# Performance work log

Measured on AMD Instinct MI355X. Metric: run time of the kernel, lower is better.

## Reference

```python
import jax, jax.numpy as jnp
import numpy as np

HEADS = 6
HEAD_DIM = 64  # channels // heads = 384 // 6
R = 2          # sparse sampler stride


def setup_inputs() -> dict:
    key = jax.random.key(0)
    k1, k2 = jax.random.split(key)
    x = jax.random.normal(k1, (8, 384, 96, 96), dtype=jnp.float32)
    # 1x1 conv weight, no bias: (out_ch=3*C, in_ch=C)
    w_qkv = jax.random.normal(k2, (1152, 384), dtype=jnp.float32) * 0.02
    return {"x": x, "w_qkv": w_qkv}


def reference(x, w_qkv):
    # sparse sampler: AvgPool2d(kernel_size=1, stride=R) == strided subsampling
    xs = x[:, :, ::R, ::R]                       # [B, C, H', W']
    B, C, H, W = xs.shape
    N = H * W
    # fused 1x1 conv producing qkv: [B, 3C, H', W']
    qkv = jnp.einsum('bchw,oc->bohw', xs, w_qkv)
    qkv = qkv.reshape(B, HEADS, 3 * HEAD_DIM, N)  # [B, h, 3d, N]
    q, k, v = jnp.split(qkv, 3, axis=2)           # each [B, h, d, N]
    # attn = (q^T @ k).softmax(-1)  -- NOTE: original forward applies no scale
    attn = jax.nn.softmax(jnp.einsum('bhdn,bhdm->bhnm', q, k), axis=-1)  # [B,h,N,N]
    # out = v @ attn^T -> [B, h, d, N]
    out = jnp.einsum('bhdm,bhnm->bhdn', v, attn)
    return out.reshape(B, C, H, W)
```

## Files before the change

### kernel.cpp

```cpp
#include <hip/hip_runtime.h>


#define NTOK 2304
#define NB 8
#define W_U16 (1152 * 384)
#define XT_U16 (NTOK * 384)
#define PLANE_U16 (NTOK * 64)
#define KVTILE_U16 8192
#define HEAD_U16 (PLANE_U16 + 36 * KVTILE_U16)
#define SLOT_U16 (XT_U16 + 6 * HEAD_U16)
#define SLOT_BYTES ((size_t)SLOT_U16 * 2)
#define WBYTES ((size_t)W_U16 * 2)
#define LOG2E 1.4426950408889634f
#define WSCALE 1024.0f
#define WS_INV (1.0f / 1024.0f)
#define SM_OFF 8.0f

typedef __attribute__((ext_vector_type(8))) _Float16 f16x8;
typedef __attribute__((ext_vector_type(4))) float f32x4;

__device__ __forceinline__ ushort f2h(float f) {
  union { _Float16 h; ushort u; } v; v.h = (_Float16)f; return v.u;
}
__device__ __forceinline__ uint cvt_pk_f16(float lo, float hi) {
  uint r;
  asm("v_cvt_pkrtz_f16_f32 %0, %1, %2" : "=v"(r) : "v"(lo), "v"(hi));
  return r;
}
__device__ __forceinline__ float exp2_fast(float x) {
  float r;
  asm("v_exp_f32 %0, %1" : "=v"(r) : "v"(x));
  return r;
}

__global__ __launch_bounds__(256) void prep_w_kernel(
    const float* __restrict__ w, ushort* __restrict__ wsu) {
  const int idx4 = blockIdx.x * 256 + threadIdx.x;
  const int o = idx4 / 96;
  const float scale = (((o % 192) < 64) ? LOG2E : 1.0f) * WSCALE;
  float4 v = *(const float4*)&w[(size_t)idx4 * 4];
  uint2 uh;
  uh.x = (uint)f2h(v.x * scale) | ((uint)f2h(v.y * scale) << 16);
  uh.y = (uint)f2h(v.z * scale) | ((uint)f2h(v.w * scale) << 16);
  *(uint2*)&wsu[(size_t)idx4 * 4] = uh;
}

__global__ __launch_bounds__(256) void prep_x_kernel(
    const float* __restrict__ x, ushort* __restrict__ wsu, int b0) {
  const int hh = blockIdx.x, cc = blockIdx.y, bb = blockIdx.z;
  const int b = b0 + bb;
  const int c0 = cc * 64;
  ushort* xth = wsu + (size_t)W_U16 + (size_t)bb * SLOT_U16;
  const float* xb = x + ((size_t)b * 384 + c0) * 9216 + 192 * hh;

  __shared__ float T[64][49];
  const int tid = threadIdx.x;
#pragma unroll
  for (int i = 0; i < 8; ++i) {
    int idx = tid + 256 * i;
    int cl = idx >> 5, q = idx & 31;
    if (q < 24) {
      float4 v = *(const float4*)&xb[(size_t)cl * 9216 + 4 * q];
      T[cl][2 * q] = v.x;
      T[cl][2 * q + 1] = v.z;
    }
  }
  __syncthreads();
#pragma unroll
  for (int i = 0; i < 2; ++i) {
    int item = tid + 256 * i;
    if (item < 384) {
      int ww = item >> 3, cg = item & 7;
      int n = hh * 48 + ww;
      uint uh[4];
#pragma unroll
      for (int p = 0; p < 4; ++p) {
        float f0 = T[8 * cg + 2 * p][ww], f1 = T[8 * cg + 2 * p + 1][ww];
        uh[p] = (uint)f2h(f0) | ((uint)f2h(f1) << 16);
      }
      uint4 H = {uh[0], uh[1], uh[2], uh[3]};
      *(uint4*)&xth[(size_t)n * 384 + c0 + 8 * cg] = H;
    }
  }
}

__global__ __launch_bounds__(256) void qkv_mfma_kernel(
    const ushort* __restrict__ wsu, int b0) {
  const int nT = blockIdx.x, oT = blockIdx.y, bb = blockIdx.z;
  const ushort* whi = wsu;
  const ushort* slot = wsu + (size_t)W_U16 + (size_t)bb * SLOT_U16;
  const ushort* xth = slot;
  const int oBase = oT * 64, nBase = nT * 64;

  __shared__ __align__(16) ushort Wh[64 * 64];
  __shared__ __align__(16) ushort Xh[64 * 64];

  const int tid = threadIdx.x;
  const int w = tid >> 6, l = tid & 63;
  const int lq = l & 15, lh = l >> 4;

  const int r0 = tid >> 3, g0 = tid & 7;
  const size_t srcA = (size_t)(oBase + r0) * 384 + 8 * g0;
  const size_t srcB = (size_t)(nBase + r0) * 384 + 8 * g0;
  const int dst0 = r0 * 64 + 8 * (g0 ^ (r0 & 7));
  const int dst1 = dst0 + 2048;

  f32x4 acc[4];
#pragma unroll
  for (int f = 0; f < 4; ++f) acc[f] = (f32x4){0.f, 0.f, 0.f, 0.f};

  uint4 t0, t1, t2, t3;
#define QSTAGE(c0)                                                        \
  {                                                                       \
    t0 = *(const uint4*)&whi[srcA + (c0)];                                \
    t1 = *(const uint4*)&whi[srcA + 32 * 384 + (c0)];                     \
    t2 = *(const uint4*)&xth[srcB + (c0)];                                \
    t3 = *(const uint4*)&xth[srcB + 32 * 384 + (c0)];                     \
  }
#define QCOMMIT()                                                         \
  {                                                                       \
    *(uint4*)&Wh[dst0] = t0; *(uint4*)&Wh[dst1] = t1;                     \
    *(uint4*)&Xh[dst0] = t2; *(uint4*)&Xh[dst1] = t3;                     \
  }

  QSTAGE(0)
  for (int step = 0; step < 6; ++step) {
    QCOMMIT()
    __syncthreads();
    if (step < 5) QSTAGE((step + 1) * 64)
    __builtin_amdgcn_s_setprio(1);
#pragma unroll
    for (int s = 0; s < 2; ++s) {
      const int nrow = 16 * w + lq;
      const int g = 4 * s + lh;
      f16x8 xh = *(const f16x8*)&Xh[nrow * 64 + 8 * (g ^ (nrow & 7))];
#pragma unroll
      for (int f = 0; f < 4; ++f) {
        const int orow = 16 * f + lq;
        f16x8 wh_ = *(const f16x8*)&Wh[orow * 64 + 8 * (g ^ (orow & 7))];
        acc[f] = __builtin_amdgcn_mfma_f32_16x16x32_f16(wh_, xh, acc[f], 0, 0, 0);
      }
    }
    __builtin_amdgcn_s_setprio(0);
    __syncthreads();
  }

  const int t = oT % 3, head = oT / 3;
  ushort* pb = (ushort*)slot + (size_t)XT_U16 + (size_t)head * HEAD_U16;
  if (t == 0) {
    const int n = nBase + 16 * w + lq;
#pragma unroll
    for (int f = 0; f < 4; ++f) {
      uint2 uh;
      uh.x = (uint)f2h(acc[f][0] * WS_INV) | ((uint)f2h(acc[f][1] * WS_INV) << 16);
      uh.y = (uint)f2h(acc[f][2] * WS_INV) | ((uint)f2h(acc[f][3] * WS_INV) << 16);
      *(uint2*)&pb[(size_t)n * 64 + 16 * f + 4 * lh] = uh;
    }
  } else if (t == 1) {
    ushort* kv = pb + (size_t)PLANE_U16 + (size_t)nT * KVTILE_U16;
    const int row = 16 * w + lq;
#pragma unroll
    for (int f = 0; f < 4; ++f) {
      uint2 uh;
      uh.x = (uint)f2h(acc[f][0] * WS_INV) | ((uint)f2h(acc[f][1] * WS_INV) << 16);
      uh.y = (uint)f2h(acc[f][2] * WS_INV) | ((uint)f2h(acc[f][3] * WS_INV) << 16);
      const int idx = row * 64 + 8 * ((2 * f + (lh >> 1)) ^ (row & 7)) + 4 * (lh & 1);
      *(uint2*)&kv[idx] = uh;
    }
  } else {
    ushort* pv = pb + (size_t)PLANE_U16 + (size_t)nT * KVTILE_U16 + 4096;
    const int col = 16 * w + lq;
    const int cg = col >> 3, cr = col & 7;
#pragma unroll
    for (int f = 0; f < 4; ++f)
#pragma unroll
      for (int r = 0; r < 4; ++r) {
        const int row = 16 * f + 4 * lh + r;
        pv[row * 64 + 8 * (cg ^ (row & 7)) + cr] = f2h(acc[f][r] * WS_INV);
      }
  }
}

__global__ __launch_bounds__(256, 5) void attn_mfma_kernel(
    const ushort* __restrict__ wsu, float* __restrict__ out, int b0, int nbw) {
  int wid = blockIdx.x + 36 * (blockIdx.y + 6 * blockIdx.z);
  const int nwg = 36 * 6 * nbw;
  if ((nwg & 7) == 0) {
    const int chunk = nwg >> 3;
    wid = (wid & 7) * chunk + (wid >> 3);
  }
  const int qt = wid % 36;
  const int rest = wid / 36;
  const int h = rest % 6;
  const int bb = rest / 6;
  const int b = b0 + bb;

  const ushort* pbh = wsu + (size_t)W_U16 + (size_t)bb * SLOT_U16 +
                      (size_t)XT_U16 + (size_t)h * HEAD_U16;
  const ushort* qhP = pbh;
  const char* kvG = (const char*)(pbh + (size_t)PLANE_U16);
  const int n0 = qt * 64;

  __shared__ __align__(16) ushort KV[8192];
  __shared__ __align__(16) ushort Pw[4][16 * 64];

  const int tid = threadIdx.x;
  const int w = tid >> 6;
  const int l = tid & 63;
  const int lq = l & 15;
  const int lh = l >> 4;

  f16x8 qh[2];
  {
    const int qrow = n0 + 16 * w + lq;
    const ushort* qr = qhP + (size_t)qrow * 64 + 8 * lh;
    qh[0] = *(const f16x8*)(qr);
    qh[1] = *(const f16x8*)(qr + 32);
  }

  f32x4 oac[4];
#pragma unroll
  for (int i = 0; i < 4; ++i) oac[i] = (f32x4){0.f, 0.f, 0.f, 0.f};
  float l_lane = 0.f;

  const char* gbase = kvG + w * 4096 + l * 16;
  char* lbase = (char*)&KV[0] + w * 4096 + l * 16;

  uint4 s0, s1, s2, s3;
#define ASTAGE(mt)                                                        \
  {                                                                       \
    const char* p_ = gbase + (size_t)(mt) * 16384;                        \
    s0 = *(const uint4*)(p_);                                             \
    s1 = *(const uint4*)(p_ + 1024);                                      \
    s2 = *(const uint4*)(p_ + 2048);                                      \
    s3 = *(const uint4*)(p_ + 3072);                                      \
  }
#define ACOMMIT()                                                         \
  {                                                                       \
    *(uint4*)(lbase) = s0;                                                \
    *(uint4*)(lbase + 1024) = s1;                                         \
    *(uint4*)(lbase + 2048) = s2;                                         \
    *(uint4*)(lbase + 3072) = s3;                                         \
  }

  ASTAGE(0)
  ACOMMIT()
  __syncthreads();

  const ushort* Kh = &KV[0];
  const ushort* Vh = &KV[4096];

  for (int mt = 0; mt < 36; ++mt) {
    const bool hasNext = (mt + 1 < 36);
    if (hasNext) ASTAGE(mt + 1)

    f32x4 st[4];
#pragma unroll
    for (int f = 0; f < 4; ++f) st[f] = (f32x4){0.f, 0.f, 0.f, 0.f};
    __builtin_amdgcn_s_setprio(1);
#pragma unroll
    for (int f = 0; f < 4; ++f) {
#pragma unroll
      for (int s = 0; s < 2; ++s) {
        const int row = 16 * f + lq;
        const int g = 4 * s + lh;
        f16x8 kh = *(const f16x8*)&Kh[row * 64 + 8 * (g ^ (row & 7))];
        st[f] = __builtin_amdgcn_mfma_f32_16x16x32_f16(kh, qh[s], st[f], 0, 0, 0);
      }
    }
    __builtin_amdgcn_s_setprio(0);

#pragma unroll
    for (int f = 0; f < 4; ++f)
#pragma unroll
      for (int r = 0; r < 4; ++r) {
        st[f][r] = exp2_fast(st[f][r] - SM_OFF);
        l_lane += st[f][r];
      }

    ushort* pw = &Pw[w][0];
#pragma unroll
    for (int f = 0; f < 4; ++f) {
      uint2 uu;
      uu.x = cvt_pk_f16(st[f][0], st[f][1]);
      uu.y = cvt_pk_f16(st[f][2], st[f][3]);
      int ui = lq * 64 + 8 * ((2 * f + (lh >> 1)) ^ (lq & 7)) + 4 * (lh & 1);
      *(uint2*)&pw[ui] = uu;
    }
    f16x8 pbf[2];
#pragma unroll
    for (int s = 0; s < 2; ++s)
      pbf[s] = *(const f16x8*)&pw[lq * 64 + 8 * ((4 * s + lh) ^ (lq & 7))];

    __builtin_amdgcn_s_setprio(1);
#pragma unroll
    for (int fd = 0; fd < 4; ++fd) {
#pragma unroll
      for (int s = 0; s < 2; ++s) {
        const int row = 16 * fd + lq;
        const int g = 4 * s + lh;
        f16x8 av = *(const f16x8*)&Vh[row * 64 + 8 * (g ^ (row & 7))];
        oac[fd] = __builtin_amdgcn_mfma_f32_16x16x32_f16(av, pbf[s], oac[fd], 0, 0, 0);
      }
    }
    __builtin_amdgcn_s_setprio(0);

    if (hasNext) {
      __syncthreads();
      ACOMMIT()
      __syncthreads();
    }
  }

  float lt = l_lane;
  lt += __shfl_xor(lt, 16);
  lt += __shfl_xor(lt, 32);
  const float inv = 1.f / lt;

  const int ncol = n0 + 16 * w + lq;
#pragma unroll
  for (int fd = 0; fd < 4; ++fd)
#pragma unroll
    for (int r = 0; r < 4; ++r)
      out[((size_t)b * 384 + h * 64 + 16 * fd + 4 * lh + r) * NTOK + ncol] =
          oac[fd][r] * inv;
}

extern "C" void kernel_launch(void* const* d_in, const int* in_sizes, int n_in,
                              void* d_out, int out_size, void* d_ws,
                              size_t ws_size, hipStream_t stream) {
  const float* x = (const float*)d_in[0];
  const float* w = (const float*)d_in[1];
  float* out = (float*)d_out;
  ushort* wsu = (ushort*)d_ws;

  int nbFit = (int)((ws_size - WBYTES) / SLOT_BYTES);
  if (nbFit < 1) nbFit = 1;
  if (nbFit > NB) nbFit = NB;

  hipLaunchKernelGGL(prep_w_kernel, dim3(432), dim3(256), 0, stream, w, wsu);
  for (int b0 = 0; b0 < NB; b0 += nbFit) {
    int nb = NB - b0;
    if (nb > nbFit) nb = nbFit;
    hipLaunchKernelGGL(prep_x_kernel, dim3(48, 6, nb), dim3(256), 0, stream,
                       x, wsu, b0);
    hipLaunchKernelGGL(qkv_mfma_kernel, dim3(36, 18, nb), dim3(256), 0, stream,
                       wsu, b0);
    hipLaunchKernelGGL(attn_mfma_kernel, dim3(36, 6, nb), dim3(256), 0, stream,
                       wsu, out, b0, nb);
  }
}
```

Baseline: 147.5 us.

## Split key range across waves, load K/V directly to registers, reduce in LDS

Each wave now handles all 64 queries of the block, but only a quarter of the key tiles. K and V fragments are read straight from global memory into registers instead of being staged through shared memory with barriers. Partial output accumulators and row sums are combined across waves through an LDS reduction at the end. The K/V producer layout drops the XOR swizzle to suit the direct global fragment reads. This removes the per-tile __syncthreads and LDS staging, at the cost of many more accumulator registers (launch bounds lowered to 2) and an extra reduction pass.

Result: slower. 177.9 us (+20.6%).

```diff
diff --git a/kernel.cpp b/kernel.cpp
--- a/kernel.cpp
+++ b/kernel.cpp
@@ -158,30 +158,26 @@
     }
   } else if (t == 1) {
     ushort* kv = pb + (size_t)PLANE_U16 + (size_t)nT * KVTILE_U16;
-    const int row = 16 * w + lq;
+    const int key = 16 * w + lq;
 #pragma unroll
     for (int f = 0; f < 4; ++f) {
       uint2 uh;
       uh.x = (uint)f2h(acc[f][0] * WS_INV) | ((uint)f2h(acc[f][1] * WS_INV) << 16);
       uh.y = (uint)f2h(acc[f][2] * WS_INV) | ((uint)f2h(acc[f][3] * WS_INV) << 16);
-      const int idx = row * 64 + 8 * ((2 * f + (lh >> 1)) ^ (row & 7)) + 4 * (lh & 1);
-      *(uint2*)&kv[idx] = uh;
+      *(uint2*)&kv[key * 64 + 16 * f + 4 * lh] = uh;
     }
   } else {
     ushort* pv = pb + (size_t)PLANE_U16 + (size_t)nT * KVTILE_U16 + 4096;
-    const int col = 16 * w + lq;
-    const int cg = col >> 3, cr = col & 7;
+    const int key = 16 * w + lq;
 #pragma unroll
     for (int f = 0; f < 4; ++f)
 #pragma unroll
-      for (int r = 0; r < 4; ++r) {
-        const int row = 16 * f + 4 * lh + r;
-        pv[row * 64 + 8 * (cg ^ (row & 7)) + cr] = f2h(acc[f][r] * WS_INV);
-      }
-  }
-}
-
-__global__ __launch_bounds__(256, 5) void attn_mfma_kernel(
+      for (int r = 0; r < 4; ++r)
+        pv[(16 * f + 4 * lh + r) * 64 + key] = f2h(acc[f][r] * WS_INV);
+  }
+}
+
+__global__ __launch_bounds__(256, 2) void attn_mfma_kernel(
     const ushort* __restrict__ wsu, float* __restrict__ out, int b0, int nbw) {
   int wid = blockIdx.x + 36 * (blockIdx.y + 6 * blockIdx.z);
   const int nwg = 36 * 6 * nbw;
@@ -201,8 +197,9 @@
   const char* kvG = (const char*)(pbh + (size_t)PLANE_U16);
   const int n0 = qt * 64;
 
-  __shared__ __align__(16) ushort KV[8192];
-  __shared__ __align__(16) ushort Pw[4][16 * 64];
+  __shared__ __align__(16) ushort Pw[4][1024];
+  __shared__ float RED[4][16][64];
+  __shared__ float RedL[4][64];
 
   const int tid = threadIdx.x;
   const int w = tid >> 6;
@@ -210,112 +207,106 @@
   const int lq = l & 15;
   const int lh = l >> 4;
 
-  f16x8 qh[2];
-  {
-    const int qrow = n0 + 16 * w + lq;
-    const ushort* qr = qhP + (size_t)qrow * 64 + 8 * lh;
-    qh[0] = *(const f16x8*)(qr);
-    qh[1] = *(const f16x8*)(qr + 32);
-  }
-
-  f32x4 oac[4];
-#pragma unroll
-  for (int i = 0; i < 4; ++i) oac[i] = (f32x4){0.f, 0.f, 0.f, 0.f};
-  float l_lane = 0.f;
-
-  const char* gbase = kvG + w * 4096 + l * 16;
-  char* lbase = (char*)&KV[0] + w * 4096 + l * 16;
-
-  uint4 s0, s1, s2, s3;
-#define ASTAGE(mt)                                                        \
-  {                                                                       \
-    const char* p_ = gbase + (size_t)(mt) * 16384;                        \
-    s0 = *(const uint4*)(p_);                                             \
-    s1 = *(const uint4*)(p_ + 1024);                                      \
-    s2 = *(const uint4*)(p_ + 2048);                                      \
-    s3 = *(const uint4*)(p_ + 3072);                                      \
-  }
-#define ACOMMIT()                                                         \
-  {                                                                       \
-    *(uint4*)(lbase) = s0;                                                \
-    *(uint4*)(lbase + 1024) = s1;                                         \
-    *(uint4*)(lbase + 2048) = s2;                                         \
-    *(uint4*)(lbase + 3072) = s3;                                         \
-  }
-
-  ASTAGE(0)
-  ACOMMIT()
+  f16x8 qh[4][2];
+#pragma unroll
+  for (int qf = 0; qf < 4; ++qf) {
+    const ushort* qr = qhP + (size_t)(n0 + 16 * qf + lq) * 64 + 8 * lh;
+    qh[qf][0] = *(const f16x8*)(qr);
+    qh[qf][1] = *(const f16x8*)(qr + 32);
+  }
+
+  f32x4 oac[4][4];
+#pragma unroll
+  for (int i = 0; i < 4; ++i)
+#pragma unroll
+    for (int j = 0; j < 4; ++j) oac[i][j] = (f32x4){0.f, 0.f, 0.f, 0.f};
+  float lp[4] = {0.f, 0.f, 0.f, 0.f};
+
+  const int kRow = lq * 128 + lh * 16;
+  const char* tbase = kvG + (size_t)w * 16384 + kRow;
+
+  for (int i = 0; i < 9; ++i) {
+    f16x8 kh[4][2], vh[4][2];
+#pragma unroll
+    for (int f = 0; f < 4; ++f) {
+      kh[f][0] = *(const f16x8*)(tbase + f * 2048);
+      kh[f][1] = *(const f16x8*)(tbase + f * 2048 + 64);
+      vh[f][0] = *(const f16x8*)(tbase + 8192 + f * 2048);
+      vh[f][1] = *(const f16x8*)(tbase + 8192 + f * 2048 + 64);
+    }
+    tbase += 4 * 16384;
+
+    ushort* pw = &Pw[w][0];
+#pragma unroll
+    for (int qf = 0; qf < 4; ++qf) {
+      f32x4 st[4];
+#pragma unroll
+      for (int kf = 0; kf < 4; ++kf) st[kf] = (f32x4){0.f, 0.f, 0.f, 0.f};
+      __builtin_amdgcn_s_setprio(1);
+#pragma unroll
+      for (int kf = 0; kf < 4; ++kf) {
+        st[kf] = __builtin_amdgcn_mfma_f32_16x16x32_f16(kh[kf][0], qh[qf][0], st[kf], 0, 0, 0);
+        st[kf] = __builtin_amdgcn_mfma_f32_16x16x32_f16(kh[kf][1], qh[qf][1], st[kf], 0, 0, 0);
+      }
+      __builtin_amdgcn_s_setprio(0);
+
+#pragma unroll
+      for (int kf = 0; kf < 4; ++kf)
+#pragma unroll
+        for (int r = 0; r < 4; ++r) {
+          st[kf][r] = exp2_fast(st[kf][r] - SM_OFF);
+          lp[qf] += st[kf][r];
+        }
+
+#pragma unroll
+      for (int kf = 0; kf < 4; ++kf) {
+        uint2 uu;
+        uu.x = cvt_pk_f16(st[kf][0], st[kf][1]);
+        uu.y = cvt_pk_f16(st[kf][2], st[kf][3]);
+        int ui = lq * 64 + 8 * ((2 * kf + (lh >> 1)) ^ (lq & 7)) + 4 * (lh & 1);
+        *(uint2*)&pw[ui] = uu;
+      }
+      f16x8 pbf0 = *(const f16x8*)&pw[lq * 64 + 8 * ((lh) ^ (lq & 7))];
+      f16x8 pbf1 = *(const f16x8*)&pw[lq * 64 + 8 * ((4 + lh) ^ (lq & 7))];
+
+      __builtin_amdgcn_s_setprio(1);
+#pragma unroll
+      for (int fd = 0; fd < 4; ++fd) {
+        oac[qf][fd] = __builtin_amdgcn_mfma_f32_16x16x32_f16(vh[fd][0], pbf0, oac[qf][fd], 0, 0, 0);
+        oac[qf][fd] = __builtin_amdgcn_mfma_f32_16x16x32_f16(vh[fd][1], pbf1, oac[qf][fd], 0, 0, 0);
+      }
+      __builtin_amdgcn_s_setprio(0);
+    }
+  }
+
   __syncthreads();
-
-  const ushort* Kh = &KV[0];
-  const ushort* Vh = &KV[4096];
-
-  for (int mt = 0; mt < 36; ++mt) {
-    const bool hasNext = (mt + 1 < 36);
-    if (hasNext) ASTAGE(mt + 1)
-
-    f32x4 st[4];
-#pragma unroll
-    for (int f = 0; f < 4; ++f) st[f] = (f32x4){0.f, 0.f, 0.f, 0.f};
-    __builtin_amdgcn_s_setprio(1);
-#pragma unroll
-    for (int f = 0; f < 4; ++f) {
-#pragma unroll
-      for (int s = 0; s < 2; ++s) {
-        const int row = 16 * f + lq;
-        const int g = 4 * s + lh;
-        f16x8 kh = *(const f16x8*)&Kh[row * 64 + 8 * (g ^ (row & 7))];
-        st[f] = __builtin_amdgcn_mfma_f32_16x16x32_f16(kh, qh[s], st[f], 0, 0, 0);
-      }
-    }
-    __builtin_amdgcn_s_setprio(0);
-
-#pragma unroll
-    for (int f = 0; f < 4; ++f)
-#pragma unroll
-      for (int r = 0; r < 4; ++r) {
-        st[f][r] = exp2_fast(st[f][r] - SM_OFF);
-        l_lane += st[f][r];
-      }
-
-    ushort* pw = &Pw[w][0];
-#pragma unroll
-    for (int f = 0; f < 4; ++f) {
-      uint2 uu;
-      uu.x = cvt_pk_f16(st[f][0], st[f][1]);
-      uu.y = cvt_pk_f16(st[f][2], st[f][3]);
-      int ui = lq * 64 + 8 * ((2 * f + (lh >> 1)) ^ (lq & 7)) + 4 * (lh & 1);
-      *(uint2*)&pw[ui] = uu;
-    }
-    f16x8 pbf[2];
-#pragma unroll
-    for (int s = 0; s < 2; ++s)
-      pbf[s] = *(const f16x8*)&pw[lq * 64 + 8 * ((4 * s + lh) ^ (lq & 7))];
-
-    __builtin_amdgcn_s_setprio(1);
-#pragma unroll
-    for (int fd = 0; fd < 4; ++fd) {
-#pragma unroll
-      for (int s = 0; s < 2; ++s) {
-        const int row = 16 * fd + lq;
-        const int g = 4 * s + lh;
-        f16x8 av = *(const f16x8*)&Vh[row * 64 + 8 * (g ^ (row & 7))];
-        oac[fd] = __builtin_amdgcn_mfma_f32_16x16x32_f16(av, pbf[s], oac[fd], 0, 0, 0);
-      }
-    }
-    __builtin_amdgcn_s_setprio(0);
-
-    if (hasNext) {
-      __syncthreads();
-      ACOMMIT()
-      __syncthreads();
-    }
-  }
-
-  float lt = l_lane;
-  lt += __shfl_xor(lt, 16);
-  lt += __shfl_xor(lt, 32);
-  const float inv = 1.f / lt;
+  f32x4 oF[4];
+#pragma unroll
+  for (int j = 0; j < 4; ++j) oF[j] = (f32x4){0.f, 0.f, 0.f, 0.f};
+  float lF = 0.f;
+#pragma unroll
+  for (int r = 0; r < 4; ++r) {
+#pragma unroll
+    for (int fd = 0; fd < 4; ++fd)
+#pragma unroll
+      for (int c = 0; c < 4; ++c) RED[w][4 * fd + c][l] = oac[r][fd][c];
+    RedL[w][l] = lp[r];
+    __syncthreads();
+    if (w == r) {
+#pragma unroll
+      for (int fd = 0; fd < 4; ++fd)
+#pragma unroll
+        for (int c = 0; c < 4; ++c)
+          oF[fd][c] = RED[0][4 * fd + c][l] + RED[1][4 * fd + c][l] +
+                      RED[2][4 * fd + c][l] + RED[3][4 * fd + c][l];
+      lF = RedL[0][l] + RedL[1][l] + RedL[2][l] + RedL[3][l];
+    }
+    __syncthreads();
+  }
+
+  lF += __shfl_xor(lF, 16);
+  lF += __shfl_xor(lF, 32);
+  const float inv = 1.f / lF;
 
   const int ncol = n0 + 16 * w + lq;
 #pragma unroll
@@ -323,7 +314,7 @@
 #pragma unroll
     for (int r = 0; r < 4; ++r)
       out[((size_t)b * 384 + h * 64 + 16 * fd + 4 * lh + r) * NTOK + ncol] =
-          oac[fd][r] * inv;
+          oF[fd][r] * inv;
 }
 
 extern "C" void kernel_launch(void* const* d_in, const int* in_sizes, int n_in,
```

## Stage two KV tiles per barrier pair and drop softmax offset

Applied to the files above, without the earlier changes.

The attention loop now loads two 64-token K/V tiles per stage into a doubled LDS buffer and iterates 18 times instead of 36. This halves the number of __syncthreads pairs and widens each global prefetch to more bytes in flight. The trade-off is twice the staging registers and LDS per block, so the occupancy hint drops from 5 to 4 blocks. The constant softmax offset subtraction is also removed, which saves one subtract per score but raises the risk of fp16 overflow in P if scores become large.

New measurement: 146.1 us. Within noise of the previous version (-1.0%).

```diff
diff --git a/kernel.cpp b/kernel.cpp
--- a/kernel.cpp
+++ b/kernel.cpp
@@ -14,7 +14,6 @@
 #define LOG2E 1.4426950408889634f
 #define WSCALE 1024.0f
 #define WS_INV (1.0f / 1024.0f)
-#define SM_OFF 8.0f
 
 typedef __attribute__((ext_vector_type(8))) _Float16 f16x8;
 typedef __attribute__((ext_vector_type(4))) float f32x4;
@@ -181,7 +180,7 @@
   }
 }
 
-__global__ __launch_bounds__(256, 5) void attn_mfma_kernel(
+__global__ __launch_bounds__(256, 4) void attn_mfma_kernel(
     const ushort* __restrict__ wsu, float* __restrict__ out, int b0, int nbw) {
   int wid = blockIdx.x + 36 * (blockIdx.y + 6 * blockIdx.z);
   const int nwg = 36 * 6 * nbw;
@@ -201,8 +200,8 @@
   const char* kvG = (const char*)(pbh + (size_t)PLANE_U16);
   const int n0 = qt * 64;
 
-  __shared__ __align__(16) ushort KV[8192];
-  __shared__ __align__(16) ushort Pw[4][16 * 64];
+  __shared__ __align__(16) ushort KV[16384];
+  __shared__ __align__(16) ushort Pw[4][1024];
 
   const int tid = threadIdx.x;
   const int w = tid >> 6;
@@ -223,17 +222,21 @@
   for (int i = 0; i < 4; ++i) oac[i] = (f32x4){0.f, 0.f, 0.f, 0.f};
   float l_lane = 0.f;
 
-  const char* gbase = kvG + w * 4096 + l * 16;
-  char* lbase = (char*)&KV[0] + w * 4096 + l * 16;
-
-  uint4 s0, s1, s2, s3;
-#define ASTAGE(mt)                                                        \
+  const char* gbase = kvG + w * 8192 + l * 16;
+  char* lbase = (char*)&KV[0] + w * 8192 + l * 16;
+
+  uint4 s0, s1, s2, s3, s4, s5, s6, s7;
+#define ASTAGE(p)                                                         \
   {                                                                       \
-    const char* p_ = gbase + (size_t)(mt) * 16384;                        \
+    const char* p_ = gbase + (size_t)(p) * 32768;                         \
     s0 = *(const uint4*)(p_);                                             \
     s1 = *(const uint4*)(p_ + 1024);                                      \
     s2 = *(const uint4*)(p_ + 2048);                                      \
     s3 = *(const uint4*)(p_ + 3072);                                      \
+    s4 = *(const uint4*)(p_ + 4096);                                      \
+    s5 = *(const uint4*)(p_ + 5120);                                      \
+    s6 = *(const uint4*)(p_ + 6144);                                      \
+    s7 = *(const uint4*)(p_ + 7168);                                      \
   }
 #define ACOMMIT()                                                         \
   {                                                                       \
@@ -241,69 +244,72 @@
     *(uint4*)(lbase + 1024) = s1;                                         \
     *(uint4*)(lbase + 2048) = s2;                                         \
     *(uint4*)(lbase + 3072) = s3;                                         \
+    *(uint4*)(lbase + 4096) = s4;                                         \
+    *(uint4*)(lbase + 5120) = s5;                                         \
+    *(uint4*)(lbase + 6144) = s6;                                         \
+    *(uint4*)(lbase + 7168) = s7;                                         \
   }
 
   ASTAGE(0)
   ACOMMIT()
   __syncthreads();
 
-  const ushort* Kh = &KV[0];
-  const ushort* Vh = &KV[4096];
-
-  for (int mt = 0; mt < 36; ++mt) {
-    const bool hasNext = (mt + 1 < 36);
-    if (hasNext) ASTAGE(mt + 1)
-
-    f32x4 st[4];
-#pragma unroll
-    for (int f = 0; f < 4; ++f) st[f] = (f32x4){0.f, 0.f, 0.f, 0.f};
-    __builtin_amdgcn_s_setprio(1);
-#pragma unroll
-    for (int f = 0; f < 4; ++f) {
-#pragma unroll
-      for (int s = 0; s < 2; ++s) {
-        const int row = 16 * f + lq;
-        const int g = 4 * s + lh;
-        f16x8 kh = *(const f16x8*)&Kh[row * 64 + 8 * (g ^ (row & 7))];
-        st[f] = __builtin_amdgcn_mfma_f32_16x16x32_f16(kh, qh[s], st[f], 0, 0, 0);
-      }
-    }
-    __builtin_amdgcn_s_setprio(0);
-
-#pragma unroll
-    for (int f = 0; f < 4; ++f)
-#pragma unroll
-      for (int r = 0; r < 4; ++r) {
-        st[f][r] = exp2_fast(st[f][r] - SM_OFF);
-        l_lane += st[f][r];
-      }
-
-    ushort* pw = &Pw[w][0];
-#pragma unroll
-    for (int f = 0; f < 4; ++f) {
-      uint2 uu;
-      uu.x = cvt_pk_f16(st[f][0], st[f][1]);
-      uu.y = cvt_pk_f16(st[f][2], st[f][3]);
-      int ui = lq * 64 + 8 * ((2 * f + (lh >> 1)) ^ (lq & 7)) + 4 * (lh & 1);
-      *(uint2*)&pw[ui] = uu;
-    }
-    f16x8 pbf[2];
-#pragma unroll
-    for (int s = 0; s < 2; ++s)
-      pbf[s] = *(const f16x8*)&pw[lq * 64 + 8 * ((4 * s + lh) ^ (lq & 7))];
-
-    __builtin_amdgcn_s_setprio(1);
-#pragma unroll
-    for (int fd = 0; fd < 4; ++fd) {
-#pragma unroll
-      for (int s = 0; s < 2; ++s) {
+  for (int it = 0; it < 18; ++it) {
+    const bool hasNext = (it + 1 < 18);
+    if (hasNext) ASTAGE(it + 1)
+
+#pragma unroll
+    for (int half = 0; half < 2; ++half) {
+      const ushort* Kh = &KV[half * 8192];
+      const ushort* Vh = &KV[half * 8192 + 4096];
+
+      f32x4 st[4];
+#pragma unroll
+      for (int f = 0; f < 4; ++f) st[f] = (f32x4){0.f, 0.f, 0.f, 0.f};
+      __builtin_amdgcn_s_setprio(1);
+#pragma unroll
+      for (int f = 0; f < 4; ++f) {
+#pragma unroll
+        for (int s = 0; s < 2; ++s) {
+          const int row = 16 * f + lq;
+          const int g = 4 * s + lh;
+          f16x8 kh = *(const f16x8*)&Kh[row * 64 + 8 * (g ^ (row & 7))];
+          st[f] = __builtin_amdgcn_mfma_f32_16x16x32_f16(kh, qh[s], st[f], 0, 0, 0);
+        }
+      }
+      __builtin_amdgcn_s_setprio(0);
+
+#pragma unroll
+      for (int f = 0; f < 4; ++f)
+#pragma unroll
+        for (int r = 0; r < 4; ++r) {
+          st[f][r] = exp2_fast(st[f][r]);
+          l_lane += st[f][r];
+        }
+
+      ushort* pw = &Pw[w][0];
+#pragma unroll
+      for (int f = 0; f < 4; ++f) {
+        uint2 uu;
+        uu.x = cvt_pk_f16(st[f][0], st[f][1]);
+        uu.y = cvt_pk_f16(st[f][2], st[f][3]);
+        int ui = lq * 64 + 8 * ((2 * f + (lh >> 1)) ^ (lq & 7)) + 4 * (lh & 1);
+        *(uint2*)&pw[ui] = uu;
+      }
+      f16x8 pbf0 = *(const f16x8*)&pw[lq * 64 + 8 * ((lh) ^ (lq & 7))];
+      f16x8 pbf1 = *(const f16x8*)&pw[lq * 64 + 8 * ((4 + lh) ^ (lq & 7))];
+
+      __builtin_amdgcn_s_setprio(1);
+#pragma unroll
+      for (int fd = 0; fd < 4; ++fd) {
         const int row = 16 * fd + lq;
-        const int g = 4 * s + lh;
-        f16x8 av = *(const f16x8*)&Vh[row * 64 + 8 * (g ^ (row & 7))];
-        oac[fd] = __builtin_amdgcn_mfma_f32_16x16x32_f16(av, pbf[s], oac[fd], 0, 0, 0);
-      }
-    }
-    __builtin_amdgcn_s_setprio(0);
+        f16x8 av0 = *(const f16x8*)&Vh[row * 64 + 8 * ((lh) ^ (row & 7))];
+        f16x8 av1 = *(const f16x8*)&Vh[row * 64 + 8 * ((4 + lh) ^ (row & 7))];
+        oac[fd] = __builtin_amdgcn_mfma_f32_16x16x32_f16(av0, pbf0, oac[fd], 0, 0, 0);
+        oac[fd] = __builtin_amdgcn_mfma_f32_16x16x32_f16(av1, pbf1, oac[fd], 0, 0, 0);
+      }
+      __builtin_amdgcn_s_setprio(0);
+    }
 
     if (hasNext) {
       __syncthreads();
```

## Process two query tiles per attention block and double-buffer QKV GEMM LDS

Applied to the files above, without the earlier changes.

The attention kernel now handles 128 queries per workgroup, two 64-query subtiles per wave, so each K/V tile staged in LDS and loaded into registers serves twice as many queries. Global K/V traffic and barrier count per query drop by half, at the cost of more registers (occupancy hint lowered from 5 to 3) and half as many workgroups. The softmax offset of 8 is removed from the exp2, which changes the value range of the unnormalized weights and risks fp16 overflow in P. The QKV GEMM uses ping-pong LDS buffers, cutting one barrier per k-step.

After: 233.8 us. +58.4%, slower.

```diff
diff --git a/kernel.cpp b/kernel.cpp
--- a/kernel.cpp
+++ b/kernel.cpp
@@ -14,7 +14,6 @@
 #define LOG2E 1.4426950408889634f
 #define WSCALE 1024.0f
 #define WS_INV (1.0f / 1024.0f)
-#define SM_OFF 8.0f
 
 typedef __attribute__((ext_vector_type(8))) _Float16 f16x8;
 typedef __attribute__((ext_vector_type(4))) float f32x4;
@@ -92,8 +91,8 @@
   const ushort* xth = slot;
   const int oBase = oT * 64, nBase = nT * 64;
 
-  __shared__ __align__(16) ushort Wh[64 * 64];
-  __shared__ __align__(16) ushort Xh[64 * 64];
+  __shared__ __align__(16) ushort Wh[2][64 * 64];
+  __shared__ __align__(16) ushort Xh[2][64 * 64];
 
   const int tid = threadIdx.x;
   const int w = tid >> 6, l = tid & 63;
@@ -117,32 +116,38 @@
     t2 = *(const uint4*)&xth[srcB + (c0)];                                \
     t3 = *(const uint4*)&xth[srcB + 32 * 384 + (c0)];                     \
   }
-#define QCOMMIT()                                                         \
+#define QCOMMIT(B)                                                        \
   {                                                                       \
-    *(uint4*)&Wh[dst0] = t0; *(uint4*)&Wh[dst1] = t1;                     \
-    *(uint4*)&Xh[dst0] = t2; *(uint4*)&Xh[dst1] = t3;                     \
+    *(uint4*)&Wh[B][dst0] = t0; *(uint4*)&Wh[B][dst1] = t1;               \
+    *(uint4*)&Xh[B][dst0] = t2; *(uint4*)&Xh[B][dst1] = t3;               \
   }
 
   QSTAGE(0)
+  QCOMMIT(0)
+  __syncthreads();
+
+#pragma unroll
   for (int step = 0; step < 6; ++step) {
-    QCOMMIT()
-    __syncthreads();
+    const int cur = step & 1;
     if (step < 5) QSTAGE((step + 1) * 64)
     __builtin_amdgcn_s_setprio(1);
 #pragma unroll
     for (int s = 0; s < 2; ++s) {
       const int nrow = 16 * w + lq;
       const int g = 4 * s + lh;
-      f16x8 xh = *(const f16x8*)&Xh[nrow * 64 + 8 * (g ^ (nrow & 7))];
+      f16x8 xh = *(const f16x8*)&Xh[cur][nrow * 64 + 8 * (g ^ (nrow & 7))];
 #pragma unroll
       for (int f = 0; f < 4; ++f) {
         const int orow = 16 * f + lq;
-        f16x8 wh_ = *(const f16x8*)&Wh[orow * 64 + 8 * (g ^ (orow & 7))];
+        f16x8 wh_ = *(const f16x8*)&Wh[cur][orow * 64 + 8 * (g ^ (orow & 7))];
         acc[f] = __builtin_amdgcn_mfma_f32_16x16x32_f16(wh_, xh, acc[f], 0, 0, 0);
       }
     }
     __builtin_amdgcn_s_setprio(0);
-    __syncthreads();
+    if (step < 5) {
+      QCOMMIT(cur ^ 1)
+      __syncthreads();
+    }
   }
 
   const int t = oT % 3, head = oT / 3;
@@ -181,16 +186,16 @@
   }
 }
 
-__global__ __launch_bounds__(256, 5) void attn_mfma_kernel(
+__global__ __launch_bounds__(256, 3) void attn_mfma_kernel(
     const ushort* __restrict__ wsu, float* __restrict__ out, int b0, int nbw) {
-  int wid = blockIdx.x + 36 * (blockIdx.y + 6 * blockIdx.z);
-  const int nwg = 36 * 6 * nbw;
+  int wid = blockIdx.x + 18 * (blockIdx.y + 6 * blockIdx.z);
+  const int nwg = 18 * 6 * nbw;
   if ((nwg & 7) == 0) {
     const int chunk = nwg >> 3;
     wid = (wid & 7) * chunk + (wid >> 3);
   }
-  const int qt = wid % 36;
-  const int rest = wid / 36;
+  const int qt = wid % 18;
+  const int rest = wid / 18;
   const int h = rest % 6;
   const int bb = rest / 6;
   const int b = b0 + bb;
@@ -199,10 +204,10 @@
                       (size_t)XT_U16 + (size_t)h * HEAD_U16;
   const ushort* qhP = pbh;
   const char* kvG = (const char*)(pbh + (size_t)PLANE_U16);
-  const int n0 = qt * 64;
+  const int n0 = qt * 128;
 
   __shared__ __align__(16) ushort KV[8192];
-  __shared__ __align__(16) ushort Pw[4][16 * 64];
+  __shared__ __align__(16) ushort Pw[4][2][1024];
 
   const int tid = threadIdx.x;
   const int w = tid >> 6;
@@ -210,18 +215,22 @@
   const int lq = l & 15;
   const int lh = l >> 4;
 
-  f16x8 qh[2];
+  f16x8 qh0[2], qh1[2];
   {
-    const int qrow = n0 + 16 * w + lq;
-    const ushort* qr = qhP + (size_t)qrow * 64 + 8 * lh;
-    qh[0] = *(const f16x8*)(qr);
-    qh[1] = *(const f16x8*)(qr + 32);
-  }
-
-  f32x4 oac[4];
-#pragma unroll
-  for (int i = 0; i < 4; ++i) oac[i] = (f32x4){0.f, 0.f, 0.f, 0.f};
-  float l_lane = 0.f;
+    const ushort* qr = qhP + (size_t)(n0 + 16 * w + lq) * 64 + 8 * lh;
+    qh0[0] = *(const f16x8*)(qr);
+    qh0[1] = *(const f16x8*)(qr + 32);
+    qh1[0] = *(const f16x8*)(qr + 4096);
+    qh1[1] = *(const f16x8*)(qr + 4128);
+  }
+
+  f32x4 oac0[4], oac1[4];
+#pragma unroll
+  for (int i = 0; i < 4; ++i) {
+    oac0[i] = (f32x4){0.f, 0.f, 0.f, 0.f};
+    oac1[i] = (f32x4){0.f, 0.f, 0.f, 0.f};
+  }
+  float l0 = 0.f, l1 = 0.f;
 
   const char* gbase = kvG + w * 4096 + l * 16;
   char* lbase = (char*)&KV[0] + w * 4096 + l * 16;
@@ -250,60 +259,114 @@
   const ushort* Kh = &KV[0];
   const ushort* Vh = &KV[4096];
 
+  const int rb0 = lq * 64, rb1 = (16 + lq) * 64,
+            rb2 = (32 + lq) * 64, rb3 = (48 + lq) * 64;
+  const int x0 = 8 * (lh ^ (lq & 7));
+  const int x1 = 8 * ((4 + lh) ^ (lq & 7));
+  const int pwr = lq * 64;
+
   for (int mt = 0; mt < 36; ++mt) {
     const bool hasNext = (mt + 1 < 36);
     if (hasNext) ASTAGE(mt + 1)
 
-    f32x4 st[4];
-#pragma unroll
-    for (int f = 0; f < 4; ++f) st[f] = (f32x4){0.f, 0.f, 0.f, 0.f};
-    __builtin_amdgcn_s_setprio(1);
-#pragma unroll
-    for (int f = 0; f < 4; ++f) {
-#pragma unroll
-      for (int s = 0; s < 2; ++s) {
-        const int row = 16 * f + lq;
-        const int g = 4 * s + lh;
-        f16x8 kh = *(const f16x8*)&Kh[row * 64 + 8 * (g ^ (row & 7))];
-        st[f] = __builtin_amdgcn_mfma_f32_16x16x32_f16(kh, qh[s], st[f], 0, 0, 0);
+    f16x8 k00 = *(const f16x8*)&Kh[rb0 + x0], k01 = *(const f16x8*)&Kh[rb0 + x1];
+    f16x8 k10 = *(const f16x8*)&Kh[rb1 + x0], k11 = *(const f16x8*)&Kh[rb1 + x1];
+    f16x8 k20 = *(const f16x8*)&Kh[rb2 + x0], k21 = *(const f16x8*)&Kh[rb2 + x1];
+    f16x8 k30 = *(const f16x8*)&Kh[rb3 + x0], k31 = *(const f16x8*)&Kh[rb3 + x1];
+    f16x8 v00 = *(const f16x8*)&Vh[rb0 + x0], v01 = *(const f16x8*)&Vh[rb0 + x1];
+    f16x8 v10 = *(const f16x8*)&Vh[rb1 + x0], v11 = *(const f16x8*)&Vh[rb1 + x1];
+    f16x8 v20 = *(const f16x8*)&Vh[rb2 + x0], v21 = *(const f16x8*)&Vh[rb2 + x1];
+    f16x8 v30 = *(const f16x8*)&Vh[rb3 + x0], v31 = *(const f16x8*)&Vh[rb3 + x1];
+
+    {
+      f32x4 st[4];
+#pragma unroll
+      for (int f = 0; f < 4; ++f) st[f] = (f32x4){0.f, 0.f, 0.f, 0.f};
+      __builtin_amdgcn_s_setprio(1);
+      st[0] = __builtin_amdgcn_mfma_f32_16x16x32_f16(k00, qh0[0], st[0], 0, 0, 0);
+      st[0] = __builtin_amdgcn_mfma_f32_16x16x32_f16(k01, qh0[1], st[0], 0, 0, 0);
+      st[1] = __builtin_amdgcn_mfma_f32_16x16x32_f16(k10, qh0[0], st[1], 0, 0, 0);
+      st[1] = __builtin_amdgcn_mfma_f32_16x16x32_f16(k11, qh0[1], st[1], 0, 0, 0);
+      st[2] = __builtin_amdgcn_mfma_f32_16x16x32_f16(k20, qh0[0], st[2], 0, 0, 0);
+      st[2] = __builtin_amdgcn_mfma_f32_16x16x32_f16(k21, qh0[1], st[2], 0, 0, 0);
+      st[3] = __builtin_amdgcn_mfma_f32_16x16x32_f16(k30, qh0[0], st[3], 0, 0, 0);
+      st[3] = __builtin_amdgcn_mfma_f32_16x16x32_f16(k31, qh0[1], st[3], 0, 0, 0);
+      __builtin_amdgcn_s_setprio(0);
+#pragma unroll
+      for (int f = 0; f < 4; ++f)
+#pragma unroll
+        for (int r = 0; r < 4; ++r) {
+          st[f][r] = exp2_fast(st[f][r]);
+          l0 += st[f][r];
+        }
+      ushort* pw = &Pw[w][0][0];
+#pragma unroll
+      for (int f = 0; f < 4; ++f) {
+        uint2 uu;
+        uu.x = cvt_pk_f16(st[f][0], st[f][1]);
+        uu.y = cvt_pk_f16(st[f][2], st[f][3]);
+        int ui = lq * 64 + 8 * ((2 * f + (lh >> 1)) ^ (lq & 7)) + 4 * (lh & 1);
+        *(uint2*)&pw[ui] = uu;
       }
-    }
-    __builtin_amdgcn_s_setprio(0);
-
-#pragma unroll
-    for (int f = 0; f < 4; ++f)
-#pragma unroll
-      for (int r = 0; r < 4; ++r) {
-        st[f][r] = exp2_fast(st[f][r] - SM_OFF);
-        l_lane += st[f][r];
+      asm volatile("" ::: "memory");
+      f16x8 p0 = *(const f16x8*)&pw[pwr + x0];
+      f16x8 p1 = *(const f16x8*)&pw[pwr + x1];
+      __builtin_amdgcn_s_setprio(1);
+      oac0[0] = __builtin_amdgcn_mfma_f32_16x16x32_f16(v00, p0, oac0[0], 0, 0, 0);
+      oac0[0] = __builtin_amdgcn_mfma_f32_16x16x32_f16(v01, p1, oac0[0], 0, 0, 0);
+      oac0[1] = __builtin_amdgcn_mfma_f32_16x16x32_f16(v10, p0, oac0[1], 0, 0, 0);
+      oac0[1] = __builtin_amdgcn_mfma_f32_16x16x32_f16(v11, p1, oac0[1], 0, 0, 0);
+      oac0[2] = __builtin_amdgcn_mfma_f32_16x16x32_f16(v20, p0, oac0[2], 0, 0, 0);
+      oac0[2] = __builtin_amdgcn_mfma_f32_16x16x32_f16(v21, p1, oac0[2], 0, 0, 0);
+      oac0[3] = __builtin_amdgcn_mfma_f32_16x16x32_f16(v30, p0, oac0[3], 0, 0, 0);
+      oac0[3] = __builtin_amdgcn_mfma_f32_16x16x32_f16(v31, p1, oac0[3], 0, 0, 0);
+      __builtin_amdgcn_s_setprio(0);
+    }
+
+    {
+      f32x4 st[4];
+#pragma unroll
+      for (int f = 0; f < 4; ++f) st[f] = (f32x4){0.f, 0.f, 0.f, 0.f};
+      __builtin_amdgcn_s_setprio(1);
+      st[0] = __builtin_amdgcn_mfma_f32_16x16x32_f16(k00, qh1[0], st[0], 0, 0, 0);
+      st[0] = __builtin_amdgcn_mfma_f32_16x16x32_f16(k01, qh1[1], st[0], 0, 0, 0);
+      st[1] = __builtin_amdgcn_mfma_f32_16x16x32_f16(k10, qh1[0], st[1], 0, 0, 0);
+      st[1] = __builtin_amdgcn_mfma_f32_16x16x32_f16(k11, qh1[1], st[1], 0, 0, 0);
+      st[2] = __builtin_amdgcn_mfma_f32_16x16x32_f16(k20, qh1[0], st[2], 0, 0, 0);
+      st[2] = __builtin_amdgcn_mfma_f32_16x16x32_f16(k21, qh1[1], st[2], 0, 0, 0);
+      st[3] = __builtin_amdgcn_mfma_f32_16x16x32_f16(k30, qh1[0], st[3], 0, 0, 0);
+      st[3] = __builtin_amdgcn_mfma_f32_16x16x32_f16(k31, qh1[1], st[3], 0, 0, 0);
+      __builtin_amdgcn_s_setprio(0);
+#pragma unroll
+      for (int f = 0; f < 4; ++f)
+#pragma unroll
+        for (int r = 0; r < 4; ++r) {
+          st[f][r] = exp2_fast(st[f][r]);
+          l1 += st[f][r];
+        }
+      ushort* pw = &Pw[w][1][0];
+#pragma unroll
+      for (int f = 0; f < 4; ++f) {
+        uint2 uu;
+        uu.x = cvt_pk_f16(st[f][0], st[f][1]);
+        uu.y = cvt_pk_f16(st[f][2], st[f][3]);
+        int ui = lq * 64 + 8 * ((2 * f + (lh >> 1)) ^ (lq & 7)) + 4 * (lh & 1);
+        *(uint2*)&pw[ui] = uu;
       }
-
-    ushort* pw = &Pw[w][0];
-#pragma unroll
-    for (int f = 0; f < 4; ++f) {
-      uint2 uu;
-      uu.x = cvt_pk_f16(st[f][0], st[f][1]);
-      uu.y = cvt_pk_f16(st[f][2], st[f][3]);
-      int ui = lq * 64 + 8 * ((2 * f + (lh >> 1)) ^ (lq & 7)) + 4 * (lh & 1);
-      *(uint2*)&pw[ui] = uu;
-    }
-    f16x8 pbf[2];
-#pragma unroll
-    for (int s = 0; s < 2; ++s)
-      pbf[s] = *(const f16x8*)&pw[lq * 64 + 8 * ((4 * s + lh) ^ (lq & 7))];
-
-    __builtin_amdgcn_s_setprio(1);
-#pragma unroll
-    for (int fd = 0; fd < 4; ++fd) {
-#pragma unroll
-      for (int s = 0; s < 2; ++s) {
-        const int row = 16 * fd + lq;
-        const int g = 4 * s + lh;
-        f16x8 av = *(const f16x8*)&Vh[row * 64 + 8 * (g ^ (row & 7))];
-        oac[fd] = __builtin_amdgcn_mfma_f32_16x16x32_f16(av, pbf[s], oac[fd], 0, 0, 0);
-      }
-    }
-    __builtin_amdgcn_s_setprio(0);
+      asm volatile("" ::: "memory");
+      f16x8 p0 = *(const f16x8*)&pw[pwr + x0];
+      f16x8 p1 = *(const f16x8*)&pw[pwr + x1];
+      __builtin_amdgcn_s_setprio(1);
+      oac1[0] = __builtin_amdgcn_mfma_f32_16x16x32_f16(v00, p0, oac1[0], 0, 0, 0);
+      oac1[0] = __builtin_amdgcn_mfma_f32_16x16x32_f16(v01, p1, oac1[0], 0, 0, 0);
+      oac1[1] = __builtin_amdgcn_mfma_f32_16x16x32_f16(v10, p0, oac1[1], 0, 0, 0);
+      oac1[1] = __builtin_amdgcn_mfma_f32_16x16x32_f16(v11, p1, oac1[1], 0, 0, 0);
+      oac1[2] = __builtin_amdgcn_mfma_f32_16x16x32_f16(v20, p0, oac1[2], 0, 0, 0);
+      oac1[2] = __builtin_amdgcn_mfma_f32_16x16x32_f16(v21, p1, oac1[2], 0, 0, 0);
+      oac1[3] = __builtin_amdgcn_mfma_f32_16x16x32_f16(v30, p0, oac1[3], 0, 0, 0);
+      oac1[3] = __builtin_amdgcn_mfma_f32_16x16x32_f16(v31, p1, oac1[3], 0, 0, 0);
+      __builtin_amdgcn_s_setprio(0);
+    }
 
     if (hasNext) {
       __syncthreads();
@@ -312,18 +375,21 @@
     }
   }
 
-  float lt = l_lane;
-  lt += __shfl_xor(lt, 16);
-  lt += __shfl_xor(lt, 32);
-  const float inv = 1.f / lt;
-
-  const int ncol = n0 + 16 * w + lq;
+  l0 += __shfl_xor(l0, 16);
+  l0 += __shfl_xor(l0, 32);
+  l1 += __shfl_xor(l1, 16);
+  l1 += __shfl_xor(l1, 32);
+  const float inv0 = 1.f / l0, inv1 = 1.f / l1;
+
+  const int ncol0 = n0 + 16 * w + lq;
 #pragma unroll
   for (int fd = 0; fd < 4; ++fd)
 #pragma unroll
-    for (int r = 0; r < 4; ++r)
-      out[((size_t)b * 384 + h * 64 + 16 * fd + 4 * lh + r) * NTOK + ncol] =
-          oac[fd][r] * inv;
+    for (int r = 0; r < 4; ++r) {
+      const size_t rowOff = ((size_t)b * 384 + h * 64 + 16 * fd + 4 * lh + r) * NTOK;
+      out[rowOff + ncol0] = oac0[fd][r] * inv0;
+      out[rowOff + ncol0 + 64] = oac1[fd][r] * inv1;
+    }
 }
 
 extern "C" void kernel_launch(void* const* d_in, const int* in_sizes, int n_in,
@@ -346,7 +412,7 @@
                        x, wsu, b0);
     hipLaunchKernelGGL(qkv_mfma_kernel, dim3(36, 18, nb), dim3(256), 0, stream,
                        wsu, b0);
-    hipLaunchKernelGGL(attn_mfma_kernel, dim3(36, 6, nb), dim3(256), 0, stream,
+    hipLaunchKernelGGL(attn_mfma_kernel, dim3(18, 6, nb), dim3(256), 0, stream,
                        wsu, out, b0, nb);
   }
 }
```
